# Kernel tuning notes

Hardware: AMD Instinct MI355X
Metric: run time of the kernel (lower is better)

The kernel has to match this reference:

```python
import jax, jax.numpy as jnp
import numpy as np
from jax import lax

KERNEL_SIZE = 5
PADDING = 2
EPS = 1e-6

def _fixed_kernels():
    # kernel_size == 5 branch of the torch module
    kv = np.zeros((5, 5), np.float32)
    kv[0, 2], kv[1, 2], kv[3, 2], kv[4, 2] = -10.0, -1.0, 1.0, 10.0
    kh = kv.T.copy()  # horizontal kernel is the transpose of the vertical one
    return jnp.asarray(kv), jnp.asarray(kh)


def setup_inputs() -> dict:
    key = jax.random.key(0)
    x = jax.random.normal(key, (16, 2, 1024, 1024), dtype=jnp.float32)
    kernel_v, kernel_h = _fixed_kernels()
    return {"x": x, "kernel_v": kernel_v, "kernel_h": kernel_h}


def _depthwise(x, k2d):
    # x: [B, C, H, W]; k2d: [5, 5]. Same 5x5 kernel applied per channel
    # (equivalent to torch's per-slice single-channel conv2d calls).
    C = x.shape[1]
    w = jnp.broadcast_to(k2d, (C, 1, KERNEL_SIZE, KERNEL_SIZE))  # OIHW, groups=C
    return lax.conv_general_dilated(
        x, w,
        window_strides=(1, 1),
        padding=[(PADDING, PADDING), (PADDING, PADDING)],
        dimension_numbers=("NCHW", "OIHW", "NCHW"),
        feature_group_count=C,
    )


def reference(x, kernel_v, kernel_h):
    x_v = _depthwise(x, kernel_v)
    x_h = _depthwise(x, kernel_h)
    return jnp.sqrt(x_v * x_v + x_h * x_h + EPS)
```

## Files before the change

### kernel.cpp

```cpp
#include <hip/hip_runtime.h>

#define H_DIM 1024
#define W_DIM 1024
#define EPS 1e-6f
#define R_ROWS 16

typedef float vfloat4 __attribute__((ext_vector_type(4)));


__global__ __launch_bounds__(256) void grad_mag_kernel(
    const float* __restrict__ x, float* __restrict__ out) {
    const int tid  = threadIdx.x;
    const int lane = tid & 63;
    const int w0   = tid * 4;
    const int h0   = blockIdx.y * R_ROWS;
    const size_t planeOff = (size_t)blockIdx.z * (size_t)(H_DIM * W_DIM);
    const float* __restrict__ xp = x + planeOff;
    float*       __restrict__ op = out + planeOff;

    float4 win[5];

    auto loadRow = [&](int h, float4& v) {
        if (h >= 0 && h < H_DIM) {
            v = *reinterpret_cast<const float4*>(xp + (size_t)h * W_DIM + w0);
        } else {
            v = make_float4(0.f, 0.f, 0.f, 0.f);
        }
    };

    loadRow(h0 - 2, win[0]);
    loadRow(h0 - 1, win[1]);
    loadRow(h0 + 0, win[2]);
    loadRow(h0 + 1, win[3]);

    #pragma unroll
    for (int i = 0; i < R_ROWS; ++i) {
        loadRow(h0 + i + 2, win[(i + 4) % 5]);

        const float4 m2 = win[(i + 0) % 5];
        const float4 m1 = win[(i + 1) % 5];
        const float4 c  = win[(i + 2) % 5];
        const float4 p1 = win[(i + 3) % 5];
        const float4 p2 = win[(i + 4) % 5];

        float wl2 = __shfl_up(c.z, 1);
        float wl1 = __shfl_up(c.w, 1);
        float wr4 = __shfl_down(c.x, 1);
        float wr5 = __shfl_down(c.y, 1);
        if (lane == 0) {
            const float* row = xp + (size_t)(h0 + i) * W_DIM;
            wl2 = (w0 >= 2) ? row[w0 - 2] : 0.f;
            wl1 = (w0 >= 1) ? row[w0 - 1] : 0.f;
        }
        if (lane == 63) {
            const float* row = xp + (size_t)(h0 + i) * W_DIM;
            wr4 = (w0 + 4 < W_DIM) ? row[w0 + 4] : 0.f;
            wr5 = (w0 + 5 < W_DIM) ? row[w0 + 5] : 0.f;
        }

        float4 xv;
        xv.x = -10.f * m2.x - m1.x + p1.x + 10.f * p2.x;
        xv.y = -10.f * m2.y - m1.y + p1.y + 10.f * p2.y;
        xv.z = -10.f * m2.z - m1.z + p1.z + 10.f * p2.z;
        xv.w = -10.f * m2.w - m1.w + p1.w + 10.f * p2.w;

        float4 xh;
        xh.x = -10.f * wl2 - wl1 + c.y + 10.f * c.z;
        xh.y = -10.f * wl1 - c.x + c.z + 10.f * c.w;
        xh.z = -10.f * c.x - c.y + c.w + 10.f * wr4;
        xh.w = -10.f * c.y - c.z + wr4 + 10.f * wr5;

        vfloat4 o;
        o.x = sqrtf(xv.x * xv.x + xh.x * xh.x + EPS);
        o.y = sqrtf(xv.y * xv.y + xh.y * xh.y + EPS);
        o.z = sqrtf(xv.z * xv.z + xh.z * xh.z + EPS);
        o.w = sqrtf(xv.w * xv.w + xh.w * xh.w + EPS);

        __builtin_nontemporal_store(
            o, reinterpret_cast<vfloat4*>(op + (size_t)(h0 + i) * W_DIM + w0));
    }
}

extern "C" void kernel_launch(void* const* d_in, const int* in_sizes, int n_in,
                              void* d_out, int out_size, void* d_ws, size_t ws_size,
                              hipStream_t stream) {
    const float* x   = (const float*)d_in[0];
    float*       out = (float*)d_out;
    const int planes = in_sizes[0] / (H_DIM * W_DIM);

    dim3 block(256, 1, 1);
    dim3 grid(1, H_DIM / R_ROWS, planes);
    grad_mag_kernel<<<grid, block, 0, stream>>>(x, out);
}
```

Measured before the change: 51.87 us.

## Preload all input rows upfront with a branch-free interior path and halve rows per block

Each block now handles 8 output rows instead of 16 and loads all 12 needed input rows into registers before computing, rather than streaming one row per iteration through a rolling window. Blocks away from the top and bottom edges skip the per-row bounds checks. This puts more loads in flight per thread and doubles the number of blocks to hide memory latency. The cost is more register use and a larger halo overhead: 12 input rows per 8 output rows instead of 20 per 16.

```diff
diff --git a/kernel.cpp b/kernel.cpp
--- a/kernel.cpp
+++ b/kernel.cpp
@@ -3,7 +3,8 @@
 #define H_DIM 1024
 #define W_DIM 1024
 #define EPS 1e-6f
-#define R_ROWS 16
+#define R_ROWS 8
+#define N_LOAD (R_ROWS + 4)
 
 typedef float vfloat4 __attribute__((ext_vector_type(4)));
 
@@ -18,30 +19,35 @@
     const float* __restrict__ xp = x + planeOff;
     float*       __restrict__ op = out + planeOff;
 
-    float4 win[5];
+    float4 win[N_LOAD];
 
-    auto loadRow = [&](int h, float4& v) {
-        if (h >= 0 && h < H_DIM) {
-            v = *reinterpret_cast<const float4*>(xp + (size_t)h * W_DIM + w0);
-        } else {
-            v = make_float4(0.f, 0.f, 0.f, 0.f);
+    const bool interior = (h0 >= 2) && (h0 + R_ROWS + 1 < H_DIM);
+    if (interior) {
+        #pragma unroll
+        for (int r = 0; r < N_LOAD; ++r) {
+            win[r] = *reinterpret_cast<const float4*>(
+                xp + (size_t)(h0 - 2 + r) * W_DIM + w0);
         }
-    };
-
-    loadRow(h0 - 2, win[0]);
-    loadRow(h0 - 1, win[1]);
-    loadRow(h0 + 0, win[2]);
-    loadRow(h0 + 1, win[3]);
+    } else {
+        #pragma unroll
+        for (int r = 0; r < N_LOAD; ++r) {
+            const int h = h0 - 2 + r;
+            if (h >= 0 && h < H_DIM) {
+                win[r] = *reinterpret_cast<const float4*>(
+                    xp + (size_t)h * W_DIM + w0);
+            } else {
+                win[r] = make_float4(0.f, 0.f, 0.f, 0.f);
+            }
+        }
+    }
 
     #pragma unroll
     for (int i = 0; i < R_ROWS; ++i) {
-        loadRow(h0 + i + 2, win[(i + 4) % 5]);
-
-        const float4 m2 = win[(i + 0) % 5];
-        const float4 m1 = win[(i + 1) % 5];
-        const float4 c  = win[(i + 2) % 5];
-        const float4 p1 = win[(i + 3) % 5];
-        const float4 p2 = win[(i + 4) % 5];
+        const float4 m2 = win[i + 0];
+        const float4 m1 = win[i + 1];
+        const float4 c  = win[i + 2];
+        const float4 p1 = win[i + 3];
+        const float4 p2 = win[i + 4];
 
         float wl2 = __shfl_up(c.z, 1);
         float wl1 = __shfl_up(c.w, 1);
```

Result: slower. 58.35 us (+12.5%).
